# Kernel tuning notes

Measured on AMD Instinct MI355X. Metric: run time of the kernel, lower is better.

The kernel has to match this reference:

```python
import jax, jax.numpy as jnp
import numpy as np

BATCH, N_FEATURES, D_MODEL = 8192, 8192, 1024


def setup_inputs() -> dict:
    key = jax.random.key(0)
    kx, kw = jax.random.split(key)
    # x: sparse feature activations in the original (COO); dense uniform here.
    x = jax.random.uniform(kx, (BATCH, N_FEATURES), dtype=jnp.float32)
    # Xavier-normal init for W_tr [n_features, d_model].
    std = float(np.sqrt(2.0 / (N_FEATURES + D_MODEL)))
    W_tr = jax.random.normal(kw, (N_FEATURES, D_MODEL), dtype=jnp.float32) * std
    bias = jnp.zeros((N_FEATURES,), dtype=jnp.float32)
    return {"x": x, "W_tr": W_tr, "bias": bias}


def reference(x, W_tr, bias):
    # h = x @ W_tr              : [B, n_features] @ [n_features, d_model] -> [B, d_model]
    # out = relu(h @ W_tr.T + b): [B, d_model] @ [d_model, n_features] -> [B, n_features]
    h = jnp.einsum("bf,fd->bd", x, W_tr)
    return jax.nn.relu(jnp.einsum("bd,fd->bf", h, W_tr) + bias)
```

## Files before the change

### kernel.cpp

```cpp
#include <hip/hip_runtime.h>
#include <hip/hip_bf16.h>
#include <stdint.h>

#define BATCH  8192
#define NFEAT  8192
#define DMODEL 1024

typedef unsigned short u16;
typedef __attribute__((ext_vector_type(8))) short  short8;
typedef __attribute__((ext_vector_type(4))) float  f32x4;

__device__ __forceinline__ u16 f2b(float f) {
    uint32_t u = __float_as_uint(f);
    u += 0x7fffu + ((u >> 16) & 1u);
    return (u16)(u >> 16);
}

__device__ __forceinline__ void gld16(const u16* g, void* l) {
    __builtin_amdgcn_global_load_lds(
        (const __attribute__((address_space(1))) void*)(uintptr_t)g,
        (__attribute__((address_space(3))) void*)(uint32_t)(uintptr_t)l,
        16, 0, 0);
}


__global__ void cvt_x_kernel(const float* __restrict__ x, u16* __restrict__ xb) {
    int i = blockIdx.x * blockDim.x + threadIdx.x;
    const float4* xv = (const float4*)x;
    float4 a = xv[2 * i];
    float4 b = xv[2 * i + 1];
    union { u16 u[8]; uint4 v; } o;
    o.u[0] = f2b(a.x); o.u[1] = f2b(a.y); o.u[2] = f2b(a.z); o.u[3] = f2b(a.w);
    o.u[4] = f2b(b.x); o.u[5] = f2b(b.y); o.u[6] = f2b(b.z); o.u[7] = f2b(b.w);
    ((uint4*)xb)[i] = o.v;
}

__global__ void cvt_w_kernel(const float* __restrict__ W,
                             u16* __restrict__ wb, u16* __restrict__ wt) {
    __shared__ u16 tile[64][65];
    const int f0 = blockIdx.x * 64;
    const int d0 = blockIdx.y * 64;
    const int t  = threadIdx.x;
#pragma unroll
    for (int rep = 0; rep < 16; ++rep) {
        int idx = rep * 256 + t;
        int r = idx >> 6, c = idx & 63;
        float v = W[(size_t)(f0 + r) * DMODEL + d0 + c];
        u16 u = f2b(v);
        tile[r][c] = u;
        wb[(size_t)(f0 + r) * DMODEL + d0 + c] = u;
    }
    __syncthreads();
#pragma unroll
    for (int rep = 0; rep < 16; ++rep) {
        int idx = rep * 256 + t;
        int r = idx >> 6, c = idx & 63;
        wt[(size_t)(d0 + r) * NFEAT + f0 + c] = tile[c][r];
    }
}

#define SYNC_IN()  do { __builtin_amdgcn_s_barrier(); \
                        asm volatile("s_waitcnt lgkmcnt(0)" ::: "memory"); } while (0)
#define SYNC_OUT() do { __builtin_amdgcn_s_setprio(0); __builtin_amdgcn_s_barrier(); } while (0)

__global__ __launch_bounds__(512, 2)
void gemm1_8phase(const u16* __restrict__ A, const u16* __restrict__ B,
                  u16* __restrict__ H, int N, int K) {
    const int NT = K >> 6;
    __shared__ __align__(1024) char lds[131072];
    const int BOFF = 98304;

    const int tid  = threadIdx.x;
    const int lane = tid & 63;
    const int wave = tid >> 6;
    const int wm   = wave >> 2;
    const int wn   = wave & 3;

    const int nwg = gridDim.x;
    const int swz = (blockIdx.x & 7) * (nwg >> 3) + (blockIdx.x >> 3);
    const int ntn = N >> 7;
    const int tm0 = (swz / ntn) << 8;
    const int tn0 = (swz % ntn) << 7;

    const int srl = lane >> 2;
    const int sch = (lane & 3) ^ (((lane >> 5) & 1) << 1);
    const int scol  = (wave & 1) * 32 + sch * 8;
    const int srow0 = (wave >> 1) * 16 + srl;

    const u16* pa[2][2];
    pa[0][0] = A + (size_t)(tm0 + srow0)            * K + scol;
    pa[0][1] = A + (size_t)(tm0 + srow0 + 64)       * K + scol;
    pa[1][0] = A + (size_t)(tm0 + 128 + srow0)      * K + scol;
    pa[1][1] = A + (size_t)(tm0 + 128 + srow0 + 64) * K + scol;
    const u16* pb[2];
    pb[0] = B + (size_t)(tn0 + srow0)      * K + scol;
    pb[1] = B + (size_t)(tn0 + srow0 + 64) * K + scol;

    auto STAGE_A = [&](int tau, int half) {
        if (tau < NT) {
            char* d = lds + (tau % 3) * 32768 + half * 16384 + wave * 1024;
            gld16(pa[half][0] + (size_t)tau * 64, d);
            gld16(pa[half][1] + (size_t)tau * 64, d + 8192);
        }
    };
    auto STAGE_B = [&](int tau) {
        if (tau < NT) {
            char* d = lds + BOFF + (tau & 1) * 16384 + wave * 1024;
            gld16(pb[0] + (size_t)tau * 64, d);
            gld16(pb[1] + (size_t)tau * 64, d + 8192);
        }
    };

    const int l15 = lane & 15, lhi = lane >> 4;
    const int pch = lhi ^ (((lane >> 3) & 1) << 1);
    const int lof = l15 * 64 + pch * 16;

    short8 a[4][2];
    short8 b[2][2];
    f32x4  acc[8][2] = {};

    const char* Ab;
    const char* Bb;
    auto LDA_ = [&](int mh) {
#pragma unroll
        for (int fm = 0; fm < 4; ++fm)
#pragma unroll
            for (int ks = 0; ks < 2; ++ks)
                a[fm][ks] = *(const short8*)(Ab + ((mh * 4 + fm) * 2 + ks) * 1024);
    };
    auto LDB_ = [&](int nh) {
#pragma unroll
        for (int ks = 0; ks < 2; ++ks)
            b[nh][ks] = *(const short8*)(Bb + (nh * 2 + ks) * 1024);
    };
    auto MMA_ = [&](int mh, int nh) {
#pragma unroll
        for (int ks = 0; ks < 2; ++ks)
#pragma unroll
            for (int fm = 0; fm < 4; ++fm)
                acc[mh * 4 + fm][nh] = __builtin_amdgcn_mfma_f32_16x16x32_bf16(
                    a[fm][ks], b[nh][ks], acc[mh * 4 + fm][nh], 0, 0, 0);
    };

    STAGE_A(0, 0); STAGE_A(0, 1); STAGE_B(0);
    STAGE_A(1, 0); STAGE_A(1, 1); STAGE_B(1);
    asm volatile("s_waitcnt vmcnt(6)" ::: "memory");
    __builtin_amdgcn_s_barrier();

    for (int t = 0; t < NT; ++t) {
        Ab = lds + (t % 3) * 32768 + wm * 16384 + lof;
        Bb = lds + BOFF + (t & 1) * 16384 + wn * 4096 + lof;

        LDA_(0); LDB_(0);
        STAGE_A(t + 2, 0);
        SYNC_IN();
        __builtin_amdgcn_s_setprio(1);
        MMA_(0, 0);
        SYNC_OUT();

        LDB_(1);
        STAGE_A(t + 2, 1);
        SYNC_IN();
        __builtin_amdgcn_s_setprio(1);
        MMA_(0, 1);
        SYNC_OUT();

        LDA_(1);
        STAGE_B(t + 2);
        SYNC_IN();
        __builtin_amdgcn_s_setprio(1);
        MMA_(1, 1);
        SYNC_OUT();

        __builtin_amdgcn_s_barrier();
        __builtin_amdgcn_s_setprio(1);
        MMA_(1, 0);
        __builtin_amdgcn_s_setprio(0);
        if (t < NT - 2)       asm volatile("s_waitcnt vmcnt(6)" ::: "memory");
        else if (t == NT - 2) asm volatile("s_waitcnt vmcnt(0)" ::: "memory");
        __builtin_amdgcn_s_barrier();
    }

    u16* lu = (u16*)lds;
#pragma unroll
    for (int fm = 0; fm < 8; ++fm)
#pragma unroll
        for (int nh = 0; nh < 2; ++nh) {
            const int col  = wn * 32 + nh * 16 + l15;
            const int row0 = wm * 128 + fm * 16 + lhi * 4;
#pragma unroll
            for (int r = 0; r < 4; ++r)
                lu[(row0 + r) * 128 + col] = f2b(acc[fm][nh][r]);
        }
    __syncthreads();
    const uint4* ls = (const uint4*)lds;
#pragma unroll
    for (int s = 0; s < 8; ++s) {
        int i = s * 512 + tid;
        int row = i >> 4;
        int col = (i & 15) * 8;
        *(uint4*)(H + (size_t)(tm0 + row) * N + (tn0 + col)) = ls[i];
    }
}

__global__ __launch_bounds__(512, 2)
void gemm2_persist(const u16* __restrict__ A, const u16* __restrict__ B,
                   float* __restrict__ O, const float* __restrict__ bias,
                   int N, int K) {
    __shared__ __align__(1024) char lds[163840];
    const int BOFF = 98304;
    const int TTOT = 64;

    const int tid  = threadIdx.x;
    const int lane = tid & 63;
    const int wave = tid >> 6;
    const int wm   = wave >> 2;
    const int wn   = wave & 3;

    const int bid = blockIdx.x;
    const int xcd = bid & 7;
    const int sub = (bid >> 3) & 3;
    const int mg  = bid >> 5;
    const int tn0     = ((xcd << 2) + sub) << 8;
    const int tm_base = mg << 10;

    const int srl = lane >> 2;
    const int sch = (lane & 3) ^ (((lane >> 5) & 1) << 1);
    const int scol  = (wave & 1) * 32 + sch * 8;
    const int srow0 = (wave >> 1) * 16 + srl;

    auto STAGE_A = [&](int tau, int half) {
        if (tau < TTOT) {
            char* d = lds + (tau % 3) * 32768 + half * 16384 + wave * 1024;
            const int rb = tm_base + ((tau >> 4) << 8) + half * 128 + srow0;
            const u16* p = A + (size_t)rb * K + ((tau & 15) << 6) + scol;
            gld16(p, d);
            gld16(p + (size_t)64 * K, d + 8192);
        }
    };
    auto STAGE_B = [&](int tau, int half) {
        if (tau < TTOT) {
            char* d = lds + BOFF + (tau & 1) * 32768 + half * 16384 + wave * 1024;
            const u16* p = B + (size_t)(tn0 + half * 128 + srow0) * K + ((tau & 15) << 6) + scol;
            gld16(p, d);
            gld16(p + (size_t)64 * K, d + 8192);
        }
    };

    const int l15 = lane & 15, lhi = lane >> 4;
    const int pch = lhi ^ (((lane >> 3) & 1) << 1);
    const int lof = l15 * 64 + pch * 16;

    short8 a[4][2];
    short8 b[4][2];
    f32x4  acc[8][4] = {};

    const char* Ab;
    const char* Bb;
    auto LDA_ = [&](int mh) {
#pragma unroll
        for (int fm = 0; fm < 4; ++fm)
#pragma unroll
            for (int ks = 0; ks < 2; ++ks)
                a[fm][ks] = *(const short8*)(Ab + ((mh * 4 + fm) * 2 + ks) * 1024);
    };
    auto LDB_ = [&](int nh) {
#pragma unroll
        for (int fn = 0; fn < 2; ++fn)
#pragma unroll
            for (int ks = 0; ks < 2; ++ks)
                b[nh * 2 + fn][ks] = *(const short8*)(Bb + (((wn & 1) * 4 + nh * 2 + fn) * 2 + ks) * 1024);
    };
    auto MMA_ = [&](int mh, int nh) {
#pragma unroll
        for (int ks = 0; ks < 2; ++ks)
#pragma unroll
            for (int fm = 0; fm < 4; ++fm)
#pragma unroll
                for (int fn = 0; fn < 2; ++fn)
                    acc[mh * 4 + fm][nh * 2 + fn] = __builtin_amdgcn_mfma_f32_16x16x32_bf16(
                        a[fm][ks], b[nh * 2 + fn][ks], acc[mh * 4 + fm][nh * 2 + fn], 0, 0, 0);
    };

    const int ocol = tn0 + wn * 64;
    float bv[4];
#pragma unroll
    for (int fn = 0; fn < 4; ++fn) bv[fn] = bias[ocol + fn * 16 + l15];

    STAGE_A(0, 0); STAGE_A(0, 1); STAGE_B(0, 0); STAGE_B(0, 1);
    STAGE_A(1, 0); STAGE_A(1, 1); STAGE_B(1, 0); STAGE_B(1, 1);
    asm volatile("s_waitcnt vmcnt(8)" ::: "memory");
    __builtin_amdgcn_s_barrier();

    for (int tt = 0; tt < TTOT; ++tt) {
        Ab = lds + (tt % 3) * 32768 + wm * 16384 + lof;
        Bb = lds + BOFF + (tt & 1) * 32768 + (wn >> 1) * 16384 + lof;

        LDA_(0); LDB_(0);
        STAGE_A(tt + 2, 0);
        asm volatile("s_waitcnt lgkmcnt(8)" ::: "memory");
        SYNC_IN();
        __builtin_amdgcn_s_setprio(1);
        MMA_(0, 0);
        SYNC_OUT();

        LDB_(1);
        STAGE_A(tt + 2, 1);
        SYNC_IN();
        __builtin_amdgcn_s_setprio(1);
        MMA_(0, 1);
        SYNC_OUT();

        LDA_(1);
        STAGE_B(tt + 2, 0);
        SYNC_IN();
        __builtin_amdgcn_s_setprio(1);
        MMA_(1, 1);
        SYNC_OUT();

        STAGE_B(tt + 2, 1);
        __builtin_amdgcn_s_barrier();
        asm volatile("s_waitcnt lgkmcnt(0)" ::: "memory");
        __builtin_amdgcn_s_setprio(1);
        MMA_(1, 0);
        __builtin_amdgcn_s_setprio(0);
        if (tt < TTOT - 2)       asm volatile("s_waitcnt vmcnt(8)" ::: "memory");
        else if (tt == TTOT - 2) asm volatile("s_waitcnt vmcnt(0)" ::: "memory");
        __builtin_amdgcn_s_barrier();

        if ((tt & 15) == 15) {
            const int orow = tm_base + ((tt >> 4) << 8) + wm * 128;
#pragma unroll
            for (int fm = 0; fm < 8; ++fm) {
                const int row0 = orow + fm * 16 + lhi * 4;
#pragma unroll
                for (int fn = 0; fn < 4; ++fn) {
                    const int col = ocol + fn * 16 + l15;
#pragma unroll
                    for (int r = 0; r < 4; ++r) {
                        float v = acc[fm][fn][r] + bv[fn];
                        O[(size_t)(row0 + r) * N + col] = v > 0.f ? v : 0.f;
                        acc[fm][fn][r] = 0.f;
                    }
                }
            }
        }
    }
}


extern "C" void kernel_launch(void* const* d_in, const int* in_sizes, int n_in,
                              void* d_out, int out_size, void* d_ws, size_t ws_size,
                              hipStream_t stream) {
    const float* x    = (const float*)d_in[0];
    const float* W    = (const float*)d_in[1];
    const float* bias = (const float*)d_in[2];
    float* out = (float*)d_out;

    char* ws = (char*)d_ws;
    u16* xb = (u16*)ws;
    u16* wt = (u16*)(ws + 134217728);
    u16* wb = (u16*)(ws + 134217728 + 16777216);
    u16* hb = (u16*)(ws + 134217728 + 2 * 16777216);

    cvt_x_kernel<<<(BATCH * NFEAT / 8) / 256, 256, 0, stream>>>(x, xb);
    cvt_w_kernel<<<dim3(NFEAT / 64, DMODEL / 64), 256, 0, stream>>>(W, wb, wt);

    gemm1_8phase<<<dim3((BATCH / 256) * (DMODEL / 128)), 512, 0, stream>>>(
        xb, wt, hb, DMODEL, NFEAT);

    gemm2_persist<<<dim3(256), 512, 0, stream>>>(
        hb, wb, out, bias, NFEAT, DMODEL);
}
```

Measured before the change: 393.7 us.

## Fuse x fp32-to-bf16 conversion into first GEMM's register-staged A pipeline

Removes the standalone conversion kernel for x and has the first GEMM load fp32 x into registers, convert it to bf16, and write it into double-buffered LDS. B tiles still use async global-to-LDS loads. This avoids writing and re-reading a full bf16 copy of x, along with one kernel launch. In exchange each GEMM block reads fp32 A data, which is twice the bytes per tile, and holds extra staging registers, which may pressure occupancy at 512 threads with two blocks per CU.

```diff
diff --git a/kernel.cpp b/kernel.cpp
--- a/kernel.cpp
+++ b/kernel.cpp
@@ -23,17 +23,6 @@
         16, 0, 0);
 }
 
-
-__global__ void cvt_x_kernel(const float* __restrict__ x, u16* __restrict__ xb) {
-    int i = blockIdx.x * blockDim.x + threadIdx.x;
-    const float4* xv = (const float4*)x;
-    float4 a = xv[2 * i];
-    float4 b = xv[2 * i + 1];
-    union { u16 u[8]; uint4 v; } o;
-    o.u[0] = f2b(a.x); o.u[1] = f2b(a.y); o.u[2] = f2b(a.z); o.u[3] = f2b(a.w);
-    o.u[4] = f2b(b.x); o.u[5] = f2b(b.y); o.u[6] = f2b(b.z); o.u[7] = f2b(b.w);
-    ((uint4*)xb)[i] = o.v;
-}
 
 __global__ void cvt_w_kernel(const float* __restrict__ W,
                              u16* __restrict__ wb, u16* __restrict__ wt) {
@@ -64,11 +53,11 @@
 #define SYNC_OUT() do { __builtin_amdgcn_s_setprio(0); __builtin_amdgcn_s_barrier(); } while (0)
 
 __global__ __launch_bounds__(512, 2)
-void gemm1_8phase(const u16* __restrict__ A, const u16* __restrict__ B,
-                  u16* __restrict__ H, int N, int K) {
+void gemm1_fused(const float* __restrict__ X, const u16* __restrict__ B,
+                 u16* __restrict__ H, int N, int K) {
     const int NT = K >> 6;
-    __shared__ __align__(1024) char lds[131072];
-    const int BOFF = 98304;
+    __shared__ __align__(1024) char lds[98304];
+    const int BOFF = 65536;
 
     const int tid  = threadIdx.x;
     const int lane = tid & 63;
@@ -87,28 +76,46 @@
     const int scol  = (wave & 1) * 32 + sch * 8;
     const int srow0 = (wave >> 1) * 16 + srl;
 
-    const u16* pa[2][2];
-    pa[0][0] = A + (size_t)(tm0 + srow0)            * K + scol;
-    pa[0][1] = A + (size_t)(tm0 + srow0 + 64)       * K + scol;
-    pa[1][0] = A + (size_t)(tm0 + 128 + srow0)      * K + scol;
-    pa[1][1] = A + (size_t)(tm0 + 128 + srow0 + 64) * K + scol;
+    const float* px[2][2];
+    px[0][0] = X + (size_t)(tm0 + srow0)            * K + scol;
+    px[0][1] = X + (size_t)(tm0 + srow0 + 64)       * K + scol;
+    px[1][0] = X + (size_t)(tm0 + 128 + srow0)      * K + scol;
+    px[1][1] = X + (size_t)(tm0 + 128 + srow0 + 64) * K + scol;
     const u16* pb[2];
     pb[0] = B + (size_t)(tn0 + srow0)      * K + scol;
     pb[1] = B + (size_t)(tn0 + srow0 + 64) * K + scol;
 
-    auto STAGE_A = [&](int tau, int half) {
-        if (tau < NT) {
-            char* d = lds + (tau % 3) * 32768 + half * 16384 + wave * 1024;
-            gld16(pa[half][0] + (size_t)tau * 64, d);
-            gld16(pa[half][1] + (size_t)tau * 64, d + 8192);
-        }
-    };
-    auto STAGE_B = [&](int tau) {
-        if (tau < NT) {
-            char* d = lds + BOFF + (tau & 1) * 16384 + wave * 1024;
-            gld16(pb[0] + (size_t)tau * 64, d);
-            gld16(pb[1] + (size_t)tau * 64, d + 8192);
-        }
+    char* const awr = lds + wave * 1024 + lane * 16;
+
+    f32x4 rbE[8], rbO[8];
+    auto LOAD_RAW = [&](int tau, f32x4* rb) {
+#pragma unroll
+        for (int h = 0; h < 2; ++h)
+#pragma unroll
+            for (int j = 0; j < 2; ++j)
+#pragma unroll
+                for (int v = 0; v < 2; ++v)
+                    rb[h * 4 + j * 2 + v] =
+                        *(const f32x4*)(px[h][j] + (size_t)tau * 64 + v * 4);
+    };
+    auto WRITE_A = [&](int buf, const f32x4* rb) {
+#pragma unroll
+        for (int h = 0; h < 2; ++h)
+#pragma unroll
+            for (int j = 0; j < 2; ++j) {
+                union { u16 u[8]; uint4 v; } o;
+#pragma unroll
+                for (int v = 0; v < 2; ++v)
+#pragma unroll
+                    for (int e = 0; e < 4; ++e)
+                        o.u[v * 4 + e] = f2b(rb[h * 4 + j * 2 + v][e]);
+                *(uint4*)(awr + buf * 32768 + h * 16384 + j * 8192) = o.v;
+            }
+    };
+    auto STAGE_B = [&](int tau, int par) {
+        char* d = lds + BOFF + par * 16384 + wave * 1024;
+        gld16(pb[0] + (size_t)tau * 64, d);
+        gld16(pb[1] + (size_t)tau * 64, d + 8192);
     };
 
     const int l15 = lane & 15, lhi = lane >> 4;
@@ -119,20 +126,6 @@
     short8 b[2][2];
     f32x4  acc[8][2] = {};
 
-    const char* Ab;
-    const char* Bb;
-    auto LDA_ = [&](int mh) {
-#pragma unroll
-        for (int fm = 0; fm < 4; ++fm)
-#pragma unroll
-            for (int ks = 0; ks < 2; ++ks)
-                a[fm][ks] = *(const short8*)(Ab + ((mh * 4 + fm) * 2 + ks) * 1024);
-    };
-    auto LDB_ = [&](int nh) {
-#pragma unroll
-        for (int ks = 0; ks < 2; ++ks)
-            b[nh][ks] = *(const short8*)(Bb + (nh * 2 + ks) * 1024);
-    };
     auto MMA_ = [&](int mh, int nh) {
 #pragma unroll
         for (int ks = 0; ks < 2; ++ks)
@@ -142,31 +135,41 @@
                     a[fm][ks], b[nh][ks], acc[mh * 4 + fm][nh], 0, 0, 0);
     };
 
-    STAGE_A(0, 0); STAGE_A(0, 1); STAGE_B(0);
-    STAGE_A(1, 0); STAGE_A(1, 1); STAGE_B(1);
-    asm volatile("s_waitcnt vmcnt(6)" ::: "memory");
-    __builtin_amdgcn_s_barrier();
-
-    for (int t = 0; t < NT; ++t) {
-        Ab = lds + (t % 3) * 32768 + wm * 16384 + lof;
-        Bb = lds + BOFF + (t & 1) * 16384 + wn * 4096 + lof;
-
-        LDA_(0); LDB_(0);
-        STAGE_A(t + 2, 0);
-        SYNC_IN();
-        __builtin_amdgcn_s_setprio(1);
+    auto KSTEP = [&](int t, f32x4* ldst, const f32x4* wsrc, int par) {
+        const char* Ab = lds + par * 32768 + wm * 16384 + lof;
+        const char* Bb = lds + BOFF + par * 16384 + wn * 4096 + lof;
+
+        if (t + 2 < NT) LOAD_RAW(t + 2, ldst);
+#pragma unroll
+        for (int fm = 0; fm < 4; ++fm)
+#pragma unroll
+            for (int ks = 0; ks < 2; ++ks)
+                a[fm][ks] = *(const short8*)(Ab + ((0 * 4 + fm) * 2 + ks) * 1024);
+#pragma unroll
+        for (int ks = 0; ks < 2; ++ks)
+            b[0][ks] = *(const short8*)(Bb + (0 * 2 + ks) * 1024);
+        if (t + 2 < NT)      asm volatile("s_waitcnt vmcnt(10)" ::: "memory");
+        else if (t + 1 < NT) asm volatile("s_waitcnt vmcnt(2)" ::: "memory");
+        SYNC_IN();
+        __builtin_amdgcn_s_setprio(1);
+        if (t + 1 < NT) WRITE_A(par ^ 1, wsrc);
         MMA_(0, 0);
         SYNC_OUT();
 
-        LDB_(1);
-        STAGE_A(t + 2, 1);
+#pragma unroll
+        for (int ks = 0; ks < 2; ++ks)
+            b[1][ks] = *(const short8*)(Bb + (1 * 2 + ks) * 1024);
         SYNC_IN();
         __builtin_amdgcn_s_setprio(1);
         MMA_(0, 1);
         SYNC_OUT();
 
-        LDA_(1);
-        STAGE_B(t + 2);
+#pragma unroll
+        for (int fm = 0; fm < 4; ++fm)
+#pragma unroll
+            for (int ks = 0; ks < 2; ++ks)
+                a[fm][ks] = *(const short8*)(Ab + ((1 * 4 + fm) * 2 + ks) * 1024);
+        if (t + 2 < NT) STAGE_B(t + 2, par);
         SYNC_IN();
         __builtin_amdgcn_s_setprio(1);
         MMA_(1, 1);
@@ -176,9 +179,23 @@
         __builtin_amdgcn_s_setprio(1);
         MMA_(1, 0);
         __builtin_amdgcn_s_setprio(0);
-        if (t < NT - 2)       asm volatile("s_waitcnt vmcnt(6)" ::: "memory");
-        else if (t == NT - 2) asm volatile("s_waitcnt vmcnt(0)" ::: "memory");
+        if (t < NT - 2) asm volatile("s_waitcnt vmcnt(10)" ::: "memory");
+        else            asm volatile("s_waitcnt vmcnt(0)"  ::: "memory");
         __builtin_amdgcn_s_barrier();
+    };
+
+    LOAD_RAW(0, rbE);
+    STAGE_B(0, 0);
+    LOAD_RAW(1, rbO);
+    STAGE_B(1, 1);
+    asm volatile("s_waitcnt vmcnt(10)" ::: "memory");
+    WRITE_A(0, rbE);
+    asm volatile("s_waitcnt lgkmcnt(0)" ::: "memory");
+    __builtin_amdgcn_s_barrier();
+
+    for (int t = 0; t < NT; t += 2) {
+        KSTEP(t,     rbE, rbO, 0);
+        KSTEP(t + 1, rbO, rbE, 1);
     }
 
     u16* lu = (u16*)lds;
@@ -358,16 +375,14 @@
     float* out = (float*)d_out;
 
     char* ws = (char*)d_ws;
-    u16* xb = (u16*)ws;
-    u16* wt = (u16*)(ws + 134217728);
-    u16* wb = (u16*)(ws + 134217728 + 16777216);
-    u16* hb = (u16*)(ws + 134217728 + 2 * 16777216);
-
-    cvt_x_kernel<<<(BATCH * NFEAT / 8) / 256, 256, 0, stream>>>(x, xb);
+    u16* wt = (u16*)ws;
+    u16* wb = (u16*)(ws + 16777216);
+    u16* hb = (u16*)(ws + 2 * 16777216);
+
     cvt_w_kernel<<<dim3(NFEAT / 64, DMODEL / 64), 256, 0, stream>>>(W, wb, wt);
 
-    gemm1_8phase<<<dim3((BATCH / 256) * (DMODEL / 128)), 512, 0, stream>>>(
-        xb, wt, hb, DMODEL, NFEAT);
+    gemm1_fused<<<dim3((BATCH / 256) * (DMODEL / 128)), 512, 0, stream>>>(
+        x, wt, hb, DMODEL, NFEAT);
 
     gemm2_persist<<<dim3(256), 512, 0, stream>>>(
         hb, wb, out, bias, NFEAT, DMODEL);
```

Measured after the change: 464.3 us. +17.9%, slower.
